# Optimization experiments

Hardware: AMD Instinct MI355X
Metric: run time of the kernel (lower is better)

Reference implementation:

```python
import jax, jax.numpy as jnp
import numpy as np

BINS = 30
MOMENTUM = 0.75
LOSS_WEIGHT = 1.0


def setup_inputs() -> dict:
    key = jax.random.key(0)
    k1, k2 = jax.random.split(key)
    N, C = 8192, 2048
    preds = jax.random.normal(k1, (N, C), dtype=jnp.float32)
    targets = jax.random.randint(k2, (N, C), 0, 2).astype(jnp.int32)  # binary multi-hot
    acc_sum = jnp.zeros((BINS, C), dtype=jnp.float32)  # EMA histogram state
    return {"preds": preds, "targets": targets, "acc_sum": acc_sum}


def reference(preds, targets, acc_sum):
    N, C = preds.shape
    t = targets.astype(preds.dtype)

    # gradient norm g = |sigmoid(p) - t|, detached (weights carry no grad)
    g = jnp.abs(jax.nn.sigmoid(jax.lax.stop_gradient(preds)) - t)

    # bin index: edges[i] = i/BINS, so bin = floor(g*BINS), g=1.0 -> last bin (edge[-1]+=1e-6)
    bin_idx = jnp.clip(jnp.floor(g * BINS).astype(jnp.int32), 0, BINS - 1)  # [N, C]

    # per-label histogram: counts[b, c] = #examples with bin b in column c
    cols = jnp.broadcast_to(jnp.arange(C, dtype=jnp.int32)[None, :], (N, C))
    counts = jnp.zeros((BINS, C), dtype=preds.dtype).at[bin_idx, cols].add(1.0)

    # n[c] = number of non-empty bins for label c
    n = jnp.sum(counts >= 1.0, axis=0).astype(preds.dtype)  # [C]

    # EMA update of the histogram (momentum > 0 branch)
    acc_new = MOMENTUM * acc_sum + (1.0 - MOMENTUM) * counts  # [BINS, C]

    tot = jnp.asarray(float(max(N, 1.0)), preds.dtype)
    weights = tot / acc_new[bin_idx, cols]               # gather per-element density
    weights = weights / jnp.maximum(n, 1.0)[None, :]      # normalize by #valid bins
    weights = jax.lax.stop_gradient(weights)

    # BCE with logits, elementwise: softplus-style stable form
    bce = jnp.logaddexp(0.0, preds) - preds * t
    loss = jnp.mean(weights * bce)
    return loss * LOSS_WEIGHT
```

## Files before the change

kernel.cpp:

```cpp
#include <hip/hip_runtime.h>

#define BINS  30
#define NROWS 8192
#define NCOLS 2048
#define COLS_PER_BLK 256
#define ROWS_PER_BLK 128
#define YSLICES 64
#define CELLS   (BINS * NCOLS)

#define FIXED_SCALE 16384.0f
#define CNT_SHIFT   24
#define SUM_MASK    ((1u << CNT_SHIFT) - 1)

#define WS_PART  0
#define WS_BPART (YSLICES * BINS * NCOLS * 4)
#define WS_CTR   (WS_BPART + 8 * 4)

__global__ __launch_bounds__(256, 5) void k_main(
    const float* __restrict__ preds, const int* __restrict__ targets,
    unsigned int* __restrict__ part, unsigned int* __restrict__ ctr)
{
    __shared__ unsigned int H[BINS * COLS_PER_BLK];
    const int t = threadIdx.x;
    if (blockIdx.x == 0 && blockIdx.y == 0 && t == 0) atomicExch(ctr, 0u);
    #pragma unroll
    for (int i = 0; i < BINS; ++i) H[i * COLS_PER_BLK + t] = 0u;
    __syncthreads();

    const int col = blockIdx.x * COLS_PER_BLK + t;
    const int r0  = blockIdx.y * ROWS_PER_BLK;
    const float* P = preds   + (size_t)r0 * NCOLS + col;
    const int*   T = targets + (size_t)r0 * NCOLS + col;

    float pc[8]; int tc[8];
    #pragma unroll
    for (int r = 0; r < 8; ++r) { pc[r] = P[r * NCOLS]; tc[r] = T[r * NCOLS]; }

    #pragma unroll 1
    for (int batch = 0; batch < ROWS_PER_BLK / 8; ++batch) {
        float pn[8]; int tn[8];
        if (batch < ROWS_PER_BLK / 8 - 1) {
            P += 8 * NCOLS; T += 8 * NCOLS;
            #pragma unroll
            for (int r = 0; r < 8; ++r) { pn[r] = P[r * NCOLS]; tn[r] = T[r * NCOLS]; }
        }
        __builtin_amdgcn_sched_barrier(0);

        #pragma unroll
        for (int r = 0; r < 8; ++r) {
            float p  = pc[r];
            float pp = tc[r] ? -p : p;
            float e  = __expf(-fabsf(pp));
            float d  = 1.0f + e;
            float r1 = __builtin_amdgcn_rcpf(d);
            float g  = (pp >= 0.0f) ? r1 : e * r1;
            int   b  = (int)(g * 30.0f);
            b = b > (BINS - 1) ? (BINS - 1) : b;
            float bce = fmaxf(pp, 0.0f) + __logf(d);
            unsigned int pk = (1u << CNT_SHIFT)
                | (unsigned int)(bce * FIXED_SCALE + 0.5f);
            H[b * COLS_PER_BLK + t] += pk;
        }
        #pragma unroll
        for (int r = 0; r < 8; ++r) { pc[r] = pn[r]; tc[r] = tn[r]; }
    }
    __syncthreads();

    const size_t outBase = (size_t)blockIdx.y * BINS * NCOLS
                         + (size_t)blockIdx.x * COLS_PER_BLK;
    for (int i = t; i < BINS * COLS_PER_BLK; i += 256)
        part[outBase + (size_t)(i >> 8) * NCOLS + (i & 255)] = H[i];
}

__global__ __launch_bounds__(256) void k_reduce16(
    unsigned int* __restrict__ part)
{
    const int gid   = blockIdx.x * 256 + threadIdx.x;
    const int chunk = gid / CELLS;
    const int cell  = gid % CELLS;
    unsigned int* Pp = part + (size_t)(chunk * 16) * CELLS + cell;

    unsigned int c = 0u, s = 0u;
    #pragma unroll
    for (int y = 0; y < 16; ++y) {
        const unsigned int v = Pp[(size_t)y * CELLS];
        c += v >> CNT_SHIFT;
        s += v & SUM_MASK;
    }
    Pp[0]     = c;
    Pp[CELLS] = s;
}

__global__ __launch_bounds__(256) void k_tail(
    const unsigned int* __restrict__ part,
    const float* __restrict__ acc_sum,
    float* __restrict__ blockPart, unsigned int* __restrict__ ctr,
    float* __restrict__ out)
{
    __shared__ float wave_sums[4];
    const int t = threadIdx.x;
    const int c = blockIdx.x * 256 + t;

    float colsum = 0.0f;
    int n = 0;
    #pragma unroll
    for (int b = 0; b < BINS; ++b) {
        const int cell = b * NCOLS + c;
        unsigned int cu = part[(size_t) 0 * CELLS + cell]
                        + part[(size_t)16 * CELLS + cell]
                        + part[(size_t)32 * CELLS + cell]
                        + part[(size_t)48 * CELLS + cell];
        unsigned int su = part[(size_t) 1 * CELLS + cell]
                        + part[(size_t)17 * CELLS + cell]
                        + part[(size_t)33 * CELLS + cell]
                        + part[(size_t)49 * CELLS + cell];
        const float cnt = (float)cu;
        if (cnt >= 1.0f) {
            n += 1;
            float acc_new = 0.75f * acc_sum[cell] + 0.25f * cnt;
            colsum += ((float)su * (1.0f / FIXED_SCALE)) / acc_new;
        }
    }
    colsum /= (float)((n > 1 ? n : 1) * NCOLS);

    #pragma unroll
    for (int off = 32; off > 0; off >>= 1)
        colsum += __shfl_down(colsum, off, 64);
    if ((t & 63) == 0) wave_sums[t >> 6] = colsum;
    __syncthreads();

    if (t == 0) {
        const float s = wave_sums[0] + wave_sums[1] + wave_sums[2] + wave_sums[3];
        atomicExch(&blockPart[blockIdx.x], s);
        __threadfence();
        if (atomicAdd(ctr, 1u) == 7u) {
            __threadfence();
            double d = 0.0;
            #pragma unroll
            for (int i = 0; i < 8; ++i)
                d += (double)atomicAdd(&blockPart[i], 0.0f);
            out[0] = (float)d;
        }
    }
}

extern "C" void kernel_launch(void* const* d_in, const int* in_sizes, int n_in,
                              void* d_out, int out_size, void* d_ws, size_t ws_size,
                              hipStream_t stream)
{
    const float* preds   = (const float*)d_in[0];
    const int*   targets = (const int*)d_in[1];
    const float* acc_sum = (const float*)d_in[2];

    unsigned int* part = (unsigned int*)((char*)d_ws + WS_PART);
    float* blockPart   = (float*)((char*)d_ws + WS_BPART);
    unsigned int* ctr  = (unsigned int*)((char*)d_ws + WS_CTR);

    dim3 gA(NCOLS / COLS_PER_BLK, NROWS / ROWS_PER_BLK);
    k_main<<<gA, 256, 0, stream>>>(preds, targets, part, ctr);

    k_reduce16<<<(4 * CELLS) / 256, 256, 0, stream>>>(part);

    k_tail<<<NCOLS / 256, 256, 0, stream>>>(part, acc_sum, blockPart, ctr,
                                            (float*)d_out);
}
```

Measured before the change: 180.0 us.

## Split each block's rows across four waves with per-wave histograms over 64 columns

Each k_main block now covers 64 columns instead of 256. Its four waves each process 32 rows of the 128-row slice, and each wave keeps a private shared-memory histogram. The four partial histograms are summed before being written out, so the grid grows fourfold while per-thread serial work drops from 128 rows to 32. This aims to raise parallelism and occupancy and shorten each thread's serial dependency chain. The costs are narrower 256-byte column segments per wave for global loads and an extra LDS reduction step.

After: 184.3 us. 2.4% more time.

```diff
diff --git a/kernel.cpp b/kernel.cpp
--- a/kernel.cpp
+++ b/kernel.cpp
@@ -3,8 +3,9 @@
 #define BINS  30
 #define NROWS 8192
 #define NCOLS 2048
-#define COLS_PER_BLK 256
+#define COLS_PER_BLK 64
 #define ROWS_PER_BLK 128
+#define ROW_SPLIT 4
 #define YSLICES 64
 #define CELLS   (BINS * NCOLS)
 
@@ -20,26 +21,28 @@
     const float* __restrict__ preds, const int* __restrict__ targets,
     unsigned int* __restrict__ part, unsigned int* __restrict__ ctr)
 {
-    __shared__ unsigned int H[BINS * COLS_PER_BLK];
+    __shared__ unsigned int H[ROW_SPLIT * BINS * COLS_PER_BLK];
     const int t = threadIdx.x;
     if (blockIdx.x == 0 && blockIdx.y == 0 && t == 0) atomicExch(ctr, 0u);
-    #pragma unroll
-    for (int i = 0; i < BINS; ++i) H[i * COLS_PER_BLK + t] = 0u;
+    for (int i = t; i < ROW_SPLIT * BINS * COLS_PER_BLK; i += 256) H[i] = 0u;
     __syncthreads();
 
-    const int col = blockIdx.x * COLS_PER_BLK + t;
-    const int r0  = blockIdx.y * ROWS_PER_BLK;
+    const int cl = t & 63;
+    const int g  = t >> 6;
+    const int col = blockIdx.x * COLS_PER_BLK + cl;
+    const int r0  = blockIdx.y * ROWS_PER_BLK + g * 32;
     const float* P = preds   + (size_t)r0 * NCOLS + col;
     const int*   T = targets + (size_t)r0 * NCOLS + col;
+    unsigned int* Hg = &H[g * BINS * COLS_PER_BLK + cl];
 
     float pc[8]; int tc[8];
     #pragma unroll
     for (int r = 0; r < 8; ++r) { pc[r] = P[r * NCOLS]; tc[r] = T[r * NCOLS]; }
 
     #pragma unroll 1
-    for (int batch = 0; batch < ROWS_PER_BLK / 8; ++batch) {
+    for (int batch = 0; batch < 4; ++batch) {
         float pn[8]; int tn[8];
-        if (batch < ROWS_PER_BLK / 8 - 1) {
+        if (batch < 3) {
             P += 8 * NCOLS; T += 8 * NCOLS;
             #pragma unroll
             for (int r = 0; r < 8; ++r) { pn[r] = P[r * NCOLS]; tn[r] = T[r * NCOLS]; }
@@ -53,23 +56,30 @@
             float e  = __expf(-fabsf(pp));
             float d  = 1.0f + e;
             float r1 = __builtin_amdgcn_rcpf(d);
-            float g  = (pp >= 0.0f) ? r1 : e * r1;
-            int   b  = (int)(g * 30.0f);
+            float g_ = (pp >= 0.0f) ? r1 : e * r1;
+            int   b  = (int)(g_ * 30.0f);
             b = b > (BINS - 1) ? (BINS - 1) : b;
             float bce = fmaxf(pp, 0.0f) + __logf(d);
             unsigned int pk = (1u << CNT_SHIFT)
                 | (unsigned int)(bce * FIXED_SCALE + 0.5f);
-            H[b * COLS_PER_BLK + t] += pk;
+            Hg[b * COLS_PER_BLK] += pk;
         }
         #pragma unroll
         for (int r = 0; r < 8; ++r) { pc[r] = pn[r]; tc[r] = tn[r]; }
     }
     __syncthreads();
 
-    const size_t outBase = (size_t)blockIdx.y * BINS * NCOLS
+    const size_t outBase = (size_t)blockIdx.y * CELLS
                          + (size_t)blockIdx.x * COLS_PER_BLK;
-    for (int i = t; i < BINS * COLS_PER_BLK; i += 256)
-        part[outBase + (size_t)(i >> 8) * NCOLS + (i & 255)] = H[i];
+    for (int i = t; i < BINS * COLS_PER_BLK; i += 256) {
+        const int b = i >> 6;
+        const int c = i & 63;
+        unsigned int v = H[0 * BINS * COLS_PER_BLK + b * COLS_PER_BLK + c]
+                       + H[1 * BINS * COLS_PER_BLK + b * COLS_PER_BLK + c]
+                       + H[2 * BINS * COLS_PER_BLK + b * COLS_PER_BLK + c]
+                       + H[3 * BINS * COLS_PER_BLK + b * COLS_PER_BLK + c];
+        part[outBase + (size_t)b * NCOLS + c] = v;
+    }
 }
 
 __global__ __launch_bounds__(256) void k_reduce16(
```

## Split main kernel into producer/consumer waves with async global-to-LDS triple buffering

Applied to the files above, without the earlier changes.

The histogram kernel now runs 512 threads. Four producer waves stream 8-row tiles of preds and targets into a triple-buffered LDS ring using global_load_lds, while four consumer waves compute bins and BCE from LDS and update the shared histogram. This replaces the per-thread register double-buffering and aims to keep more loads in flight to hide memory latency. In exchange it adds about 48KB of LDS per block and a block-wide barrier per tile, and half the waves do no arithmetic.

Result: no change. 179.5 us (-0.3%).

```diff
diff --git a/kernel.cpp b/kernel.cpp
--- a/kernel.cpp
+++ b/kernel.cpp
@@ -12,63 +12,102 @@
 #define CNT_SHIFT   24
 #define SUM_MASK    ((1u << CNT_SHIFT) - 1)
 
+#define NBUF      3
+#define TILE_ROWS 8
+#define NTILES    (ROWS_PER_BLK / TILE_ROWS)
+
 #define WS_PART  0
 #define WS_BPART (YSLICES * BINS * NCOLS * 4)
 #define WS_CTR   (WS_BPART + 8 * 4)
 
-__global__ __launch_bounds__(256, 5) void k_main(
+#define FENCE asm volatile("" ::: "memory")
+
+__device__ __forceinline__ void gll16(const void* g, void* l)
+{
+    __builtin_amdgcn_global_load_lds(
+        (const __attribute__((address_space(1))) void*)g,
+        (__attribute__((address_space(3))) void*)l, 16, 0, 0);
+}
+
+__global__ __launch_bounds__(512, 4) void k_main(
     const float* __restrict__ preds, const int* __restrict__ targets,
     unsigned int* __restrict__ part, unsigned int* __restrict__ ctr)
 {
     __shared__ unsigned int H[BINS * COLS_PER_BLK];
-    const int t = threadIdx.x;
+    __shared__ __align__(16) float TbP[NBUF][TILE_ROWS][COLS_PER_BLK];
+    __shared__ __align__(16) int   TbT[NBUF][TILE_ROWS][COLS_PER_BLK];
+
+    const int t    = threadIdx.x;
+    const int wv   = t >> 6;
+    const int lane = t & 63;
     if (blockIdx.x == 0 && blockIdx.y == 0 && t == 0) atomicExch(ctr, 0u);
-    #pragma unroll
-    for (int i = 0; i < BINS; ++i) H[i * COLS_PER_BLK + t] = 0u;
+
+    for (int i = t; i < BINS * COLS_PER_BLK; i += 512) H[i] = 0u;
     __syncthreads();
 
-    const int col = blockIdx.x * COLS_PER_BLK + t;
-    const int r0  = blockIdx.y * ROWS_PER_BLK;
-    const float* P = preds   + (size_t)r0 * NCOLS + col;
-    const int*   T = targets + (size_t)r0 * NCOLS + col;
-
-    float pc[8]; int tc[8];
-    #pragma unroll
-    for (int r = 0; r < 8; ++r) { pc[r] = P[r * NCOLS]; tc[r] = T[r * NCOLS]; }
+    const float* Pbase = preds   + (size_t)(blockIdx.y * ROWS_PER_BLK) * NCOLS
+                                 + blockIdx.x * COLS_PER_BLK;
+    const int*   Tbase = targets + (size_t)(blockIdx.y * ROWS_PER_BLK) * NCOLS
+                                 + blockIdx.x * COLS_PER_BLK;
+
+    const bool is_prod = (wv >= 4);
+    const int  pw      = wv - 4;
+
+    auto issue = [&](int k) {
+        const int b = k % NBUF;
+        #pragma unroll
+        for (int j = 0; j < 2; ++j) {
+            const int lr  = 2 * pw + j;
+            const int row = k * TILE_ROWS + lr;
+            gll16(Pbase + (size_t)row * NCOLS + 4 * lane, &TbP[b][lr][0]);
+            gll16(Tbase + (size_t)row * NCOLS + 4 * lane, &TbT[b][lr][0]);
+        }
+    };
+
+    if (is_prod) {
+        issue(0); issue(1);
+        asm volatile("s_waitcnt vmcnt(4)" ::: "memory");
+        __builtin_amdgcn_sched_barrier(0);
+    }
+    FENCE; __builtin_amdgcn_s_barrier(); FENCE;
 
     #pragma unroll 1
-    for (int batch = 0; batch < ROWS_PER_BLK / 8; ++batch) {
-        float pn[8]; int tn[8];
-        if (batch < ROWS_PER_BLK / 8 - 1) {
-            P += 8 * NCOLS; T += 8 * NCOLS;
+    for (int k = 0; k < NTILES; ++k) {
+        if (!is_prod) {
+            const int buf = k % NBUF;
             #pragma unroll
-            for (int r = 0; r < 8; ++r) { pn[r] = P[r * NCOLS]; tn[r] = T[r * NCOLS]; }
-        }
-        __builtin_amdgcn_sched_barrier(0);
-
-        #pragma unroll
-        for (int r = 0; r < 8; ++r) {
-            float p  = pc[r];
-            float pp = tc[r] ? -p : p;
-            float e  = __expf(-fabsf(pp));
-            float d  = 1.0f + e;
-            float r1 = __builtin_amdgcn_rcpf(d);
-            float g  = (pp >= 0.0f) ? r1 : e * r1;
-            int   b  = (int)(g * 30.0f);
-            b = b > (BINS - 1) ? (BINS - 1) : b;
-            float bce = fmaxf(pp, 0.0f) + __logf(d);
-            unsigned int pk = (1u << CNT_SHIFT)
-                | (unsigned int)(bce * FIXED_SCALE + 0.5f);
-            H[b * COLS_PER_BLK + t] += pk;
-        }
-        #pragma unroll
-        for (int r = 0; r < 8; ++r) { pc[r] = pn[r]; tc[r] = tn[r]; }
-    }
+            for (int r = 0; r < TILE_ROWS; ++r) {
+                float p  = TbP[buf][r][t];
+                int   tv = TbT[buf][r][t];
+                float pp = tv ? -p : p;
+                float e  = __expf(-fabsf(pp));
+                float d  = 1.0f + e;
+                float r1 = __builtin_amdgcn_rcpf(d);
+                float g  = (pp >= 0.0f) ? r1 : e * r1;
+                int   bi = (int)(g * 30.0f);
+                bi = bi > (BINS - 1) ? (BINS - 1) : bi;
+                float bce = fmaxf(pp, 0.0f) + __logf(d);
+                unsigned int pk = (1u << CNT_SHIFT)
+                    | (unsigned int)(bce * FIXED_SCALE + 0.5f);
+                H[bi * COLS_PER_BLK + t] += pk;
+            }
+        } else {
+            if (k + 2 < NTILES) {
+                issue(k + 2);
+                asm volatile("s_waitcnt vmcnt(4)" ::: "memory");
+            } else {
+                asm volatile("s_waitcnt vmcnt(0)" ::: "memory");
+            }
+            __builtin_amdgcn_sched_barrier(0);
+        }
+        FENCE; __builtin_amdgcn_s_barrier(); FENCE;
+    }
+
     __syncthreads();
 
-    const size_t outBase = (size_t)blockIdx.y * BINS * NCOLS
+    const size_t outBase = (size_t)blockIdx.y * CELLS
                          + (size_t)blockIdx.x * COLS_PER_BLK;
-    for (int i = t; i < BINS * COLS_PER_BLK; i += 256)
+    for (int i = t; i < BINS * COLS_PER_BLK; i += 512)
         part[outBase + (size_t)(i >> 8) * NCOLS + (i & 255)] = H[i];
 }
 
@@ -157,7 +196,7 @@
     unsigned int* ctr  = (unsigned int*)((char*)d_ws + WS_CTR);
 
     dim3 gA(NCOLS / COLS_PER_BLK, NROWS / ROWS_PER_BLK);
-    k_main<<<gA, 256, 0, stream>>>(preds, targets, part, ctr);
+    k_main<<<gA, 512, 0, stream>>>(preds, targets, part, ctr);
 
     k_reduce16<<<(4 * CELLS) / 256, 256, 0, stream>>>(part);
 
```
